# Performance work log

Hardware: AMD Instinct MI355X
Metric: run time of the kernel (lower is better)

Reference implementation:

```python
import jax, jax.numpy as jnp
import numpy as np

N_E = 8192
E_DIM = 256
BETA = 0.25


def setup_inputs() -> dict:
    key = jax.random.key(0)
    k1, k2 = jax.random.split(key)
    z = jax.random.normal(k1, (4, 256, 16, 16, 16), dtype=jnp.float32)
    weight = jax.random.normal(k2, (N_E, E_DIM), dtype=jnp.float32)
    return {"z": z, "weight": weight}


def reference(z, weight):
    # b c l h w -> b l h w c
    zc = jnp.transpose(z, (0, 2, 3, 4, 1))
    zf = zc.reshape(-1, E_DIM)  # [N, D]
    n = zf.shape[0]

    # squared euclidean distances to all codes: [N, n_e]
    d = (jnp.sum(zf * zf, axis=1, keepdims=True)
         + jnp.sum(weight * weight, axis=1)
         - 2.0 * jnp.einsum('bd,nd->bn', zf, weight))
    idx = jnp.argmin(d, axis=1)  # [N] int

    z_q = weight[idx].reshape(zc.shape)  # codebook gather

    # histogram of code usage (equivalent to one-hot mean, without the NxK one-hot)
    counts = jnp.zeros((N_E,), dtype=zf.dtype).at[idx].add(1.0)
    avg_probs = counts / jnp.asarray(n, zf.dtype)
    perplexity = jnp.exp(-jnp.sum(avg_probs * jnp.log(avg_probs + 1e-10)))
    unique = jnp.sum(counts > 0).astype(jnp.int32)

    # commitment loss (z_q detached) + straight-through estimator
    loss = BETA * jnp.mean((jax.lax.stop_gradient(z_q) - zc) ** 2)
    z_q_st = zc + jax.lax.stop_gradient(z_q - zc)

    # b l h w c -> b c l h w
    z_q_out = jnp.transpose(z_q_st, (0, 4, 1, 2, 3))
    return z_q_out, loss, perplexity, unique, idx
```

## Files before the change

kernel.cpp:

```cpp
#include <hip/hip_runtime.h>

#define NQ     16384
#define EDIM   256
#define NE     8192
#define LHW    4096
#define BETA   0.25f

#define WS_WSQ    0
#define WS_CNT    32768
#define WS_LOSS   65536
#define WS_IDX    65792
#define WS_BEST   131328
#define WS_APACK  2359552
#define WS_BPACK  10748160
#define WS_NEED   14942464

typedef __attribute__((ext_vector_type(8))) short bf16x8;
typedef __attribute__((ext_vector_type(4))) float f32x4;

__device__ __forceinline__ unsigned f32_sortable(float f) {
    unsigned b = __float_as_uint(f);
    return b ^ ((unsigned)((int)b >> 31) | 0x80000000u);
}
__device__ __forceinline__ unsigned short bf16_rn(float f) {
    unsigned u = __float_as_uint(f);
    return (unsigned short)((u + 0x7FFFu + ((u >> 16) & 1u)) >> 16);
}

__global__ __launch_bounds__(256) void wsq_pack_w(const float* __restrict__ w,
                                                  float* __restrict__ wsq,
                                                  unsigned* __restrict__ Bp32,
                                                  unsigned* __restrict__ counts,
                                                  float* __restrict__ loss) {
    int wave = threadIdx.x >> 6, lane = threadIdx.x & 63;
    int row = blockIdx.x * 4 + wave;
    if (blockIdx.x < 32) {
        counts[blockIdx.x * 256 + threadIdx.x] = 0u;
        if (blockIdx.x == 0 && threadIdx.x == 0) loss[0] = 0.f;
    }
    float4 v = *(const float4*)(w + (size_t)row * EDIM + lane * 4);
    double s = (double)v.x * v.x + (double)v.y * v.y +
               (double)v.z * v.z + (double)v.w * v.w;
    unsigned p0 = (unsigned)bf16_rn(v.x) | ((unsigned)bf16_rn(v.y) << 16);
    unsigned p1 = (unsigned)bf16_rn(v.z) | ((unsigned)bf16_rn(v.w) << 16);
    *(uint2*)(Bp32 + (size_t)row * 128 + lane * 2) = make_uint2(p0, p1);
    #pragma unroll
    for (int off = 32; off; off >>= 1) s += __shfl_xor(s, off, 64);
    if (lane == 0) wsq[row] = (float)s;
}

__global__ __launch_bounds__(256) void wsq_kernel(const float* __restrict__ w,
                                                  float* __restrict__ wsq) {
    int wave = threadIdx.x >> 6, lane = threadIdx.x & 63;
    int row = blockIdx.x * 4 + wave;
    float4 v = *(const float4*)(w + (size_t)row * EDIM + lane * 4);
    double s = (double)v.x * v.x + (double)v.y * v.y +
               (double)v.z * v.z + (double)v.w * v.w;
    #pragma unroll
    for (int off = 32; off; off >>= 1) s += __shfl_xor(s, off, 64);
    if (lane == 0) wsq[row] = (float)s;
}

__global__ __launch_bounds__(1024) void pack_z(const float* __restrict__ z,
                                               unsigned* __restrict__ Ap32) {
    __shared__ unsigned lds[64 * 129];
    int tid = threadIdx.x;
    int tn = tid & 63, tc = tid >> 6;
    int n0 = blockIdx.x * 64;
    int n = n0 + tn;
    int b = n >> 12, lhw = n & 4095;
    #pragma unroll
    for (int cc = 0; cc < 16; cc += 2) {
        int d = tc * 16 + cc;
        float v0 = z[((size_t)b * EDIM + d) * LHW + lhw];
        float v1 = z[((size_t)b * EDIM + d + 1) * LHW + lhw];
        lds[tn * 129 + (d >> 1)] =
            (unsigned)bf16_rn(v0) | ((unsigned)bf16_rn(v1) << 16);
    }
    __syncthreads();
    #pragma unroll
    for (int p = 0; p < 8; ++p) {
        int flat = p * 1024 + tid;
        int row = flat >> 7, c = flat & 127;
        Ap32[(size_t)(n0 + row) * 128 + c] = lds[row * 129 + c];
    }
}

__global__ __launch_bounds__(256, 3) void dist_mfma(const unsigned short* __restrict__ Ap,
                                                    const unsigned short* __restrict__ Bp,
                                                    const float* __restrict__ wsq,
                                                    unsigned* __restrict__ s1) {
    __shared__ __align__(16) unsigned short lds_b[2][128 * 64];
    int tid = threadIdx.x, lane = tid & 63, w = tid >> 6;
    int x = blockIdx.x, nt = blockIdx.y;
    int quad = lane >> 4, col = lane & 15;
    int rsel = lane >> 3, seg = lane & 7;

    const unsigned short* arow = Ap + (size_t)(nt * 128 + w * 32 + col) * 256;
    const unsigned short* Bbase = Bp + (size_t)(x * 128) * 256;

    f32x4 acc[2][8];
    #pragma unroll
    for (int i = 0; i < 2; ++i)
        #pragma unroll
        for (int j = 0; j < 8; ++j) acc[i][j] = (f32x4){0.f, 0.f, 0.f, 0.f};

    auto stage_chunk = [&](int kc, int bsel) {
        int k0s = kc * 64;
        #pragma unroll
        for (int p = 0; p < 4; ++p) {
            int c = w * 4 + p;
            const unsigned short* gb =
                Bbase + (size_t)(c * 8 + rsel) * 256 + k0s + ((seg ^ (rsel & 7)) * 8);
            __builtin_amdgcn_global_load_lds(
                (const __attribute__((address_space(1))) void*)gb,
                (__attribute__((address_space(3))) void*)(&lds_b[bsel][c * 512]),
                16, 0, 0);
        }
    };

    stage_chunk(0, 0);

    #pragma unroll
    for (int kcc = 0; kcc < 4; ++kcc) {
        int k0 = kcc * 64;
        int cur = kcc & 1;
        bf16x8 af[2][2];
        #pragma unroll
        for (int i = 0; i < 2; ++i)
            #pragma unroll
            for (int h = 0; h < 2; ++h)
                af[i][h] = *(const bf16x8*)(arow + i * 16 * 256 + k0 + h * 32 + quad * 8);
        asm volatile("" ::: "memory");
        if (kcc < 3) {
            stage_chunk(kcc + 1, cur ^ 1);
            asm volatile("s_waitcnt vmcnt(8)" ::: "memory");
        } else {
            asm volatile("s_waitcnt vmcnt(4)" ::: "memory");
        }
        __builtin_amdgcn_s_barrier();
        asm volatile("" ::: "memory");
        __builtin_amdgcn_s_setprio(1);
        #pragma unroll
        for (int h = 0; h < 2; ++h) {
            bf16x8 bf[8];
            #pragma unroll
            for (int j = 0; j < 8; ++j)
                bf[j] = *(const bf16x8*)(&lds_b[cur][(j * 16 + col) * 64 +
                                         (((h * 4 + quad) ^ (col & 7)) * 8)]);
            #pragma unroll
            for (int i = 0; i < 2; ++i)
                #pragma unroll
                for (int j = 0; j < 8; ++j)
                    acc[i][j] = __builtin_amdgcn_mfma_f32_16x16x32_bf16(
                        af[i][h], bf[j], acc[i][j], 0, 0, 0);
        }
        __builtin_amdgcn_s_setprio(0);
        asm volatile("" ::: "memory");
        if (kcc < 3) {
            __builtin_amdgcn_s_barrier();
            asm volatile("" ::: "memory");
        }
    }

    unsigned m1[2][4], m2[2][4];
    #pragma unroll
    for (int i = 0; i < 2; ++i)
        #pragma unroll
        for (int r = 0; r < 4; ++r) { m1[i][r] = 0xFFFFFFFFu; m2[i][r] = 0xFFFFFFFFu; }
    #pragma unroll
    for (int j = 0; j < 8; ++j) {
        int e = x * 128 + j * 16 + col;
        unsigned jc = (unsigned)(j * 16 + col);
        float wq_off = wsq[e] + 4096.0f;
        #pragma unroll
        for (int i = 0; i < 2; ++i)
            #pragma unroll
            for (int r = 0; r < 4; ++r) {
                float d = fmaf(-2.0f, acc[i][j][r], wq_off);
                unsigned k = (__float_as_uint(d) & 0xFFFFFF80u) | jc;
                unsigned mx = (m1[i][r] > k) ? m1[i][r] : k;
                m1[i][r] = (m1[i][r] < k) ? m1[i][r] : k;
                m2[i][r] = (m2[i][r] < mx) ? m2[i][r] : mx;
            }
    }
    #pragma unroll
    for (int i = 0; i < 2; ++i)
        #pragma unroll
        for (int r = 0; r < 4; ++r) {
            unsigned a1 = m1[i][r], a2 = m2[i][r];
            #pragma unroll
            for (int off = 1; off < 16; off <<= 1) {
                unsigned b1 = __shfl_xor(a1, off, 64);
                unsigned b2 = __shfl_xor(a2, off, 64);
                unsigned lo1 = a1 < b1 ? a1 : b1;
                unsigned hi1 = a1 < b1 ? b1 : a1;
                unsigned lo2 = a2 < b2 ? a2 : b2;
                a1 = lo1;
                a2 = hi1 < lo2 ? hi1 : lo2;
            }
            if (col == 0) {
                int q = nt * 128 + w * 32 + i * 16 + quad * 4 + r;
                size_t o = (size_t)q * 128 + x * 2;
                s1[o] = a1; s1[o + 1] = a2;
            }
        }
}

__global__ __launch_bounds__(256) void refine_kernel(const float* __restrict__ z,
                                                     const float* __restrict__ w,
                                                     const float* __restrict__ wsq,
                                                     const unsigned* __restrict__ s1,
                                                     unsigned* __restrict__ idxarr) {
    __shared__ float lds_z[4][260];
    int tid = threadIdx.x, lane = tid & 63, wv = tid >> 6;
    int q0 = blockIdx.x * 4;
    int q = q0 + wv;
    int b = q0 >> 12, lhw0 = q0 & 4095;
    {
        float4 zc = *(const float4*)(z + ((size_t)b * EDIM + tid) * LHW + lhw0);
        lds_z[0][tid] = zc.x; lds_z[1][tid] = zc.y;
        lds_z[2][tid] = zc.z; lds_z[3][tid] = zc.w;
    }
    uint2 kk2 = *(const uint2*)(s1 + (size_t)q * 128 + lane * 2);
    unsigned long long a1 =
        ((unsigned long long)(kk2.x >> 7) << 13) | (unsigned)(lane * 128 + (kk2.x & 127u));
    unsigned long long a2 =
        ((unsigned long long)(kk2.y >> 7) << 13) | (unsigned)(lane * 128 + (kk2.y & 127u));
    #pragma unroll
    for (int off = 1; off < 8; off <<= 1) {
        unsigned long long b1 = __shfl_xor(a1, off, 64);
        unsigned long long b2 = __shfl_xor(a2, off, 64);
        unsigned long long lo1 = a1 < b1 ? a1 : b1;
        unsigned long long hi1 = a1 < b1 ? b1 : a1;
        unsigned long long lo2 = a2 < b2 ? a2 : b2;
        a1 = lo1;
        a2 = hi1 < lo2 ? hi1 : lo2;
    }
    __syncthreads();
    float zv[4];
    #pragma unroll
    for (int t = 0; t < 4; ++t)
        zv[t] = lds_z[wv][lane * 4 + t];
    unsigned long long bestk = ~0ull;
    #pragma unroll
    for (int c = 0; c < 16; ++c) {
        int src = (c >> 1) * 8;
        unsigned long long kc = (c & 1) ? __shfl(a2, src, 64) : __shfl(a1, src, 64);
        unsigned e = (unsigned)(kc & (unsigned long long)(NE - 1));
        float4 wv4 = *(const float4*)(w + (size_t)e * EDIM + lane * 4);
        float p = zv[0] * wv4.x + zv[1] * wv4.y + zv[2] * wv4.z + zv[3] * wv4.w;
        #pragma unroll
        for (int off = 32; off; off >>= 1) p += __shfl_xor(p, off, 64);
        float d = wsq[e] - 2.0f * p;
        unsigned long long key = ((unsigned long long)f32_sortable(d) << 32) | e;
        if (key < bestk) bestk = key;
    }
    if (lane == 0) idxarr[q] = (unsigned)(bestk & 0xFFFFFFFFull);
}

__global__ __launch_bounds__(256, 2) void dist_fp32(const float* __restrict__ z,
                                                    const float* __restrict__ w,
                                                    const float* __restrict__ wsq,
                                                    unsigned long long* __restrict__ best) {
    __shared__ float lds_a[32 * 128];
    __shared__ float lds_b[32 * 132];
    int tid = threadIdx.x;
    int tx = tid & 15, ty = tid >> 4;
    int n0 = blockIdx.y * 128;
    int bb_ = n0 >> 12, lhw0 = n0 & 4095;
    const float* zb = z + (size_t)bb_ * (EDIM * LHW) + lhw0;
    int ebase = blockIdx.x * 2048;
    unsigned long long runmin[8];
    #pragma unroll
    for (int i = 0; i < 8; ++i) runmin[i] = ~0ull;
    float acc[64];
    for (int et = 0; et < 16; ++et) {
        int e0 = ebase + et * 128;
        #pragma unroll
        for (int i = 0; i < 64; ++i) acc[i] = 0.f;
        for (int kc = 0; kc < 8; ++kc) {
            int k0 = kc * 32;
            #pragma unroll
            for (int p = 0; p < 4; ++p) {
                int f = p * 256 + tid;
                int kk = f >> 5, nn4 = f & 31;
                float4 v = *(const float4*)(zb + (size_t)(k0 + kk) * LHW + nn4 * 4);
                *((float4*)(lds_a + kk * 128 + nn4 * 4)) = v;
            }
            #pragma unroll
            for (int p = 0; p < 4; ++p) {
                int f = p * 256 + tid;
                int ee = f >> 3, kk4 = f & 7;
                float4 v = *(const float4*)(w + (size_t)(e0 + ee) * EDIM + k0 + kk4 * 4);
                lds_b[(kk4 * 4 + 0) * 132 + ee] = v.x;
                lds_b[(kk4 * 4 + 1) * 132 + ee] = v.y;
                lds_b[(kk4 * 4 + 2) * 132 + ee] = v.z;
                lds_b[(kk4 * 4 + 3) * 132 + ee] = v.w;
            }
            __syncthreads();
            #pragma unroll
            for (int k = 0; k < 32; ++k) {
                float a[8], bv[8];
                *(float4*)(a)      = *(float4*)(lds_a + k * 128 + ty * 8);
                *(float4*)(a + 4)  = *(float4*)(lds_a + k * 128 + ty * 8 + 4);
                *(float4*)(bv)     = *(float4*)(lds_b + k * 132 + tx * 8);
                *(float4*)(bv + 4) = *(float4*)(lds_b + k * 132 + tx * 8 + 4);
                #pragma unroll
                for (int i = 0; i < 8; ++i)
                    #pragma unroll
                    for (int j = 0; j < 8; ++j)
                        acc[i * 8 + j] = fmaf(a[i], bv[j], acc[i * 8 + j]);
            }
            __syncthreads();
        }
        #pragma unroll
        for (int i = 0; i < 8; ++i) {
            unsigned long long m = runmin[i];
            #pragma unroll
            for (int j = 0; j < 8; ++j) {
                int e = e0 + tx * 8 + j;
                float d = wsq[e] - 2.0f * acc[i * 8 + j];
                unsigned long long key =
                    ((unsigned long long)f32_sortable(d) << 32) | (unsigned)e;
                m = (m < key) ? m : key;
            }
            runmin[i] = m;
        }
    }
    #pragma unroll
    for (int i = 0; i < 8; ++i) {
        unsigned long long kk = runmin[i];
        #pragma unroll
        for (int off = 8; off >= 1; off >>= 1) {
            unsigned long long o = __shfl_xor(kk, off, 16);
            kk = (kk < o) ? kk : o;
        }
        if (tx == 0) atomicMin(&best[n0 + ty * 8 + i], kk);
    }
}

__global__ __launch_bounds__(256) void extract_idx(const unsigned long long* __restrict__ best,
                                                   unsigned* __restrict__ idxarr) {
    int n = blockIdx.x * 256 + threadIdx.x;
    idxarr[n] = (unsigned)(best[n] & 0xFFFFFFFFull) & (NE - 1);
}

__global__ __launch_bounds__(1024) void gather_kernel(const float* __restrict__ z,
                                                      const float* __restrict__ w,
                                                      const unsigned* __restrict__ idxarr,
                                                      unsigned* __restrict__ counts,
                                                      float* __restrict__ loss,
                                                      float* __restrict__ out,
                                                      float* __restrict__ out_idx) {
    __shared__ int idx_s[64];
    __shared__ float wl[64 * 257];
    __shared__ float lsum[16];
    int tid = threadIdx.x;
    int n0 = blockIdx.x * 64;
    if (tid < 64) {
        int idx = (int)(idxarr[n0 + tid] & (NE - 1));
        idx_s[tid] = idx;
        out_idx[n0 + tid] = (float)idx;
        atomicAdd(&counts[idx], 1u);
    }
    __syncthreads();
    {
        int r0 = tid >> 8, cl = tid & 255;
        #pragma unroll
        for (int i = 0; i < 16; ++i)
            wl[(r0 + i * 4) * 257 + cl] = w[(size_t)idx_s[r0 + i * 4] * EDIM + cl];
    }
    __syncthreads();
    int tn = tid & 63, tc = tid >> 6;
    int bb_ = n0 >> 12, lhw0 = n0 & 4095;
    size_t zb = (size_t)bb_ * (EDIM * LHW) + lhw0 + tn;
    float accl = 0.f;
    #pragma unroll
    for (int cc = 0; cc < 16; ++cc) {
        int c = tc * 16 + cc;
        float wv = wl[tn * 257 + c];
        size_t a = zb + (size_t)c * LHW;
        float zv = z[a];
        float diff = wv - zv;
        out[a] = zv + diff;
        accl += diff * diff;
    }
    #pragma unroll
    for (int off = 32; off; off >>= 1) accl += __shfl_xor(accl, off, 64);
    if ((tid & 63) == 0) lsum[tid >> 6] = accl;
    __syncthreads();
    if (tid < 16) {
        float v = lsum[tid];
        v += __shfl_xor(v, 8, 16);
        v += __shfl_xor(v, 4, 16);
        v += __shfl_xor(v, 2, 16);
        v += __shfl_xor(v, 1, 16);
        if (tid == 0) atomicAdd(loss, v);
    }
}

__global__ __launch_bounds__(256) void finalize_kernel(const unsigned* __restrict__ counts,
                                                       const float* __restrict__ loss,
                                                       float* __restrict__ out_scalars) {
    __shared__ float ss[4];
    __shared__ int uu[4];
    int tid = threadIdx.x;
    float s = 0.f;
    int uniq = 0;
    for (int i = tid; i < NE; i += 256) {
        unsigned c = counts[i];
        if (c > 0) {
            float p = (float)c * (1.0f / (float)NQ);
            s += p * logf(p + 1e-10f);
            uniq++;
        }
    }
    #pragma unroll
    for (int off = 32; off; off >>= 1) {
        s += __shfl_xor(s, off, 64);
        uniq += __shfl_xor(uniq, off, 64);
    }
    int wave = tid >> 6;
    if ((tid & 63) == 0) { ss[wave] = s; uu[wave] = uniq; }
    __syncthreads();
    if (tid == 0) {
        float st = ss[0] + ss[1] + ss[2] + ss[3];
        int ut = uu[0] + uu[1] + uu[2] + uu[3];
        out_scalars[0] = BETA * loss[0] * (1.0f / (float)(NQ * EDIM));
        out_scalars[1] = expf(-st);
        out_scalars[2] = (float)ut;
    }
}

extern "C" void kernel_launch(void* const* d_in, const int* in_sizes, int n_in,
                              void* d_out, int out_size, void* d_ws, size_t ws_size,
                              hipStream_t stream) {
    const float* z = (const float*)d_in[0];
    const float* w = (const float*)d_in[1];
    float* out = (float*)d_out;
    char* ws = (char*)d_ws;
    float* wsq = (float*)(ws + WS_WSQ);
    unsigned* counts = (unsigned*)(ws + WS_CNT);
    float* loss = (float*)(ws + WS_LOSS);
    unsigned* idxarr = (unsigned*)(ws + WS_IDX);
    unsigned long long* best = (unsigned long long*)(ws + WS_BEST);
    unsigned* Ap = (unsigned*)(ws + WS_APACK);
    unsigned* Bp = (unsigned*)(ws + WS_BPACK);

    int idx_off = out_size - NQ;
    int scal_off = idx_off - 3;
    float* out_idx = out + idx_off;
    float* out_scalars = out + scal_off;

    unsigned* s1 = (unsigned*)out;

    if (ws_size >= (size_t)WS_NEED) {
        wsq_pack_w<<<NE / 4, 256, 0, stream>>>(w, wsq, Bp, counts, loss);
        pack_z<<<NQ / 64, 1024, 0, stream>>>(z, Ap);
        dist_mfma<<<dim3(64, 128), 256, 0, stream>>>((const unsigned short*)Ap,
                                                     (const unsigned short*)Bp, wsq, s1);
        refine_kernel<<<NQ / 4, 256, 0, stream>>>(z, w, wsq, s1, idxarr);
    } else {
        hipMemsetAsync(counts, 0, NE * sizeof(unsigned), stream);
        hipMemsetAsync(loss, 0, sizeof(float), stream);
        wsq_kernel<<<NE / 4, 256, 0, stream>>>(w, wsq);
        hipMemsetAsync(best, 0xFF, NQ * sizeof(unsigned long long), stream);
        dist_fp32<<<dim3(4, 128), 256, 0, stream>>>(z, w, wsq, best);
        extract_idx<<<NQ / 256, 256, 0, stream>>>(best, idxarr);
    }

    gather_kernel<<<NQ / 64, 1024, 0, stream>>>(z, w, idxarr, counts, loss, out, out_idx);
    finalize_kernel<<<1, 256, 0, stream>>>(counts, loss, out_scalars);
}
```

Baseline: 237.8 us.

## Process four codebook tiles per block, overlapping argmin epilogue with next tile's MFMAs

Each dist_mfma block now walks four consecutive 128-code tiles instead of one, with double-buffered accumulators so the top-2 selection and shuffle merge of the previous tile are interleaved with the MFMA loop of the current tile. B-tile staging is pipelined continuously across tile boundaries, and the grid shrinks from 64 to 16 blocks in x. The aim is to hide the epilogue's ALU and shuffle work and the per-block ramp-up behind matrix-core work. The cost is doubled accumulator registers, which lowers the occupancy target from 3 to 2 blocks and leaves fewer blocks to fill the GPU.

```diff
diff --git a/kernel.cpp b/kernel.cpp
--- a/kernel.cpp
+++ b/kernel.cpp
@@ -86,32 +86,28 @@
     }
 }
 
-__global__ __launch_bounds__(256, 3) void dist_mfma(const unsigned short* __restrict__ Ap,
+__global__ __launch_bounds__(256, 2) void dist_mfma(const unsigned short* __restrict__ Ap,
                                                     const unsigned short* __restrict__ Bp,
                                                     const float* __restrict__ wsq,
                                                     unsigned* __restrict__ s1) {
     __shared__ __align__(16) unsigned short lds_b[2][128 * 64];
     int tid = threadIdx.x, lane = tid & 63, w = tid >> 6;
-    int x = blockIdx.x, nt = blockIdx.y;
+    int xg = blockIdx.x, nt = blockIdx.y;
     int quad = lane >> 4, col = lane & 15;
     int rsel = lane >> 3, seg = lane & 7;
 
     const unsigned short* arow = Ap + (size_t)(nt * 128 + w * 32 + col) * 256;
-    const unsigned short* Bbase = Bp + (size_t)(x * 128) * 256;
-
-    f32x4 acc[2][8];
-    #pragma unroll
-    for (int i = 0; i < 2; ++i)
-        #pragma unroll
-        for (int j = 0; j < 8; ++j) acc[i][j] = (f32x4){0.f, 0.f, 0.f, 0.f};
-
-    auto stage_chunk = [&](int kc, int bsel) {
-        int k0s = kc * 64;
+
+    f32x4 accA[2][8], accB[2][8];
+    unsigned m1[2][4], m2[2][4];
+    float wqA[8], wqB[8];
+
+    auto stage = [&](int xt, int kc, int bsel) {
         #pragma unroll
         for (int p = 0; p < 4; ++p) {
             int c = w * 4 + p;
-            const unsigned short* gb =
-                Bbase + (size_t)(c * 8 + rsel) * 256 + k0s + ((seg ^ (rsel & 7)) * 8);
+            const unsigned short* gb = Bp + (size_t)(xt * 128 + c * 8 + rsel) * 256
+                                       + kc * 64 + ((seg ^ (rsel & 7)) * 8);
             __builtin_amdgcn_global_load_lds(
                 (const __attribute__((address_space(1))) void*)gb,
                 (__attribute__((address_space(3))) void*)(&lds_b[bsel][c * 512]),
@@ -119,92 +115,134 @@
         }
     };
 
-    stage_chunk(0, 0);
-
-    #pragma unroll
-    for (int kcc = 0; kcc < 4; ++kcc) {
-        int k0 = kcc * 64;
-        int cur = kcc & 1;
-        bf16x8 af[2][2];
+    auto slice2 = [&](const f32x4 (&ap)[2][8], const float (&wqp)[8],
+                      int jbase, bool first) {
+        if (first) {
+            #pragma unroll
+            for (int i = 0; i < 2; ++i)
+                #pragma unroll
+                for (int r = 0; r < 4; ++r) { m1[i][r] = 0xFFFFFFFFu; m2[i][r] = 0xFFFFFFFFu; }
+        }
+        #pragma unroll
+        for (int jo = 0; jo < 2; ++jo) {
+            int jj = jbase + jo;
+            unsigned jc = (unsigned)(jj * 16 + col);
+            float wq = wqp[jj] + 4096.0f;
+            #pragma unroll
+            for (int i = 0; i < 2; ++i)
+                #pragma unroll
+                for (int r = 0; r < 4; ++r) {
+                    float d = fmaf(-2.0f, ap[i][jj][r], wq);
+                    unsigned kk = (__float_as_uint(d) & 0xFFFFFF80u) | jc;
+                    unsigned mx = (m1[i][r] > kk) ? m1[i][r] : kk;
+                    m1[i][r] = (m1[i][r] < kk) ? m1[i][r] : kk;
+                    m2[i][r] = (m2[i][r] < mx) ? m2[i][r] : mx;
+                }
+        }
+    };
+
+    auto merge_write = [&](int xt) {
         #pragma unroll
         for (int i = 0; i < 2; ++i)
             #pragma unroll
-            for (int h = 0; h < 2; ++h)
-                af[i][h] = *(const bf16x8*)(arow + i * 16 * 256 + k0 + h * 32 + quad * 8);
-        asm volatile("" ::: "memory");
-        if (kcc < 3) {
-            stage_chunk(kcc + 1, cur ^ 1);
-            asm volatile("s_waitcnt vmcnt(8)" ::: "memory");
-        } else {
-            asm volatile("s_waitcnt vmcnt(4)" ::: "memory");
-        }
-        __builtin_amdgcn_s_barrier();
-        asm volatile("" ::: "memory");
-        __builtin_amdgcn_s_setprio(1);
-        #pragma unroll
-        for (int h = 0; h < 2; ++h) {
-            bf16x8 bf[8];
-            #pragma unroll
-            for (int j = 0; j < 8; ++j)
-                bf[j] = *(const bf16x8*)(&lds_b[cur][(j * 16 + col) * 64 +
-                                         (((h * 4 + quad) ^ (col & 7)) * 8)]);
+            for (int r = 0; r < 4; ++r) {
+                unsigned a1 = m1[i][r], a2 = m2[i][r];
+                #pragma unroll
+                for (int off = 1; off < 16; off <<= 1) {
+                    unsigned b1 = __shfl_xor(a1, off, 64);
+                    unsigned b2 = __shfl_xor(a2, off, 64);
+                    unsigned lo1 = a1 < b1 ? a1 : b1;
+                    unsigned hi1 = a1 < b1 ? b1 : a1;
+                    unsigned lo2 = a2 < b2 ? a2 : b2;
+                    a1 = lo1;
+                    a2 = hi1 < lo2 ? hi1 : lo2;
+                }
+                if (col == 0) {
+                    int q = nt * 128 + w * 32 + i * 16 + quad * 4 + r;
+                    size_t o = (size_t)q * 128 + xt * 2;
+                    s1[o] = a1; s1[o + 1] = a2;
+                }
+            }
+    };
+
+    stage(xg * 4, 0, 0);
+
+    #pragma unroll
+    for (int t = 0; t < 4; ++t) {
+        f32x4 (&acc)[2][8]  = (t & 1) ? accB : accA;
+        f32x4 (&accp)[2][8] = (t & 1) ? accA : accB;
+        float (&wqc)[8] = (t & 1) ? wqB : wqA;
+        float (&wqp)[8] = (t & 1) ? wqA : wqB;
+        int xt = xg * 4 + t;
+        #pragma unroll
+        for (int k = 0; k < 4; ++k) {
+            int p = t * 4 + k, cur = p & 1;
+            if (k == 0) {
+                #pragma unroll
+                for (int i = 0; i < 2; ++i)
+                    #pragma unroll
+                    for (int j = 0; j < 8; ++j) acc[i][j] = (f32x4){0.f, 0.f, 0.f, 0.f};
+            }
+            bf16x8 af[2][2];
             #pragma unroll
             for (int i = 0; i < 2; ++i)
                 #pragma unroll
+                for (int h = 0; h < 2; ++h)
+                    af[i][h] = *(const bf16x8*)(arow + i * 16 * 256 + k * 64 + h * 32 + quad * 8);
+            asm volatile("" ::: "memory");
+            if (k == 3) {
+                #pragma unroll
                 for (int j = 0; j < 8; ++j)
-                    acc[i][j] = __builtin_amdgcn_mfma_f32_16x16x32_bf16(
-                        af[i][h], bf[j], acc[i][j], 0, 0, 0);
-        }
-        __builtin_amdgcn_s_setprio(0);
-        asm volatile("" ::: "memory");
-        if (kcc < 3) {
+                    wqc[j] = wsq[xt * 128 + j * 16 + col];
+                asm volatile("" ::: "memory");
+            }
+            bool last = (t == 3 && k == 3);
+            if (!last) {
+                int t2 = (k == 3) ? t + 1 : t;
+                int k2 = (k == 3) ? 0 : k + 1;
+                stage(xg * 4 + t2, k2, cur ^ 1);
+            }
+            asm volatile("" ::: "memory");
+            if (k == 3) {
+                if (t == 3) asm volatile("s_waitcnt vmcnt(12)" ::: "memory");
+                else        asm volatile("s_waitcnt vmcnt(16)" ::: "memory");
+            } else {
+                asm volatile("s_waitcnt vmcnt(8)" ::: "memory");
+            }
             __builtin_amdgcn_s_barrier();
             asm volatile("" ::: "memory");
-        }
-    }
-
-    unsigned m1[2][4], m2[2][4];
-    #pragma unroll
-    for (int i = 0; i < 2; ++i)
-        #pragma unroll
-        for (int r = 0; r < 4; ++r) { m1[i][r] = 0xFFFFFFFFu; m2[i][r] = 0xFFFFFFFFu; }
-    #pragma unroll
-    for (int j = 0; j < 8; ++j) {
-        int e = x * 128 + j * 16 + col;
-        unsigned jc = (unsigned)(j * 16 + col);
-        float wq_off = wsq[e] + 4096.0f;
-        #pragma unroll
-        for (int i = 0; i < 2; ++i)
-            #pragma unroll
-            for (int r = 0; r < 4; ++r) {
-                float d = fmaf(-2.0f, acc[i][j][r], wq_off);
-                unsigned k = (__float_as_uint(d) & 0xFFFFFF80u) | jc;
-                unsigned mx = (m1[i][r] > k) ? m1[i][r] : k;
-                m1[i][r] = (m1[i][r] < k) ? m1[i][r] : k;
-                m2[i][r] = (m2[i][r] < mx) ? m2[i][r] : mx;
-            }
-    }
-    #pragma unroll
-    for (int i = 0; i < 2; ++i)
-        #pragma unroll
-        for (int r = 0; r < 4; ++r) {
-            unsigned a1 = m1[i][r], a2 = m2[i][r];
-            #pragma unroll
-            for (int off = 1; off < 16; off <<= 1) {
-                unsigned b1 = __shfl_xor(a1, off, 64);
-                unsigned b2 = __shfl_xor(a2, off, 64);
-                unsigned lo1 = a1 < b1 ? a1 : b1;
-                unsigned hi1 = a1 < b1 ? b1 : a1;
-                unsigned lo2 = a2 < b2 ? a2 : b2;
-                a1 = lo1;
-                a2 = hi1 < lo2 ? hi1 : lo2;
-            }
-            if (col == 0) {
-                int q = nt * 128 + w * 32 + i * 16 + quad * 4 + r;
-                size_t o = (size_t)q * 128 + x * 2;
-                s1[o] = a1; s1[o + 1] = a2;
-            }
-        }
+            __builtin_amdgcn_s_setprio(1);
+            #pragma unroll
+            for (int h = 0; h < 2; ++h) {
+                bf16x8 bf[8];
+                #pragma unroll
+                for (int j = 0; j < 8; ++j)
+                    bf[j] = *(const bf16x8*)(&lds_b[cur][(j * 16 + col) * 64 +
+                                             (((h * 4 + quad) ^ (col & 7)) * 8)]);
+                #pragma unroll
+                for (int i = 0; i < 2; ++i)
+                    #pragma unroll
+                    for (int j = 0; j < 8; ++j)
+                        acc[i][j] = __builtin_amdgcn_mfma_f32_16x16x32_bf16(
+                            af[i][h], bf[j], acc[i][j], 0, 0, 0);
+            }
+            __builtin_amdgcn_s_setprio(0);
+            if (t > 0) {
+                slice2(accp, wqp, k * 2, k == 0);
+                if (k == 3) merge_write(xt - 1);
+            }
+            __builtin_amdgcn_sched_barrier(0);
+            asm volatile("" ::: "memory");
+            if (!last) {
+                __builtin_amdgcn_s_barrier();
+                asm volatile("" ::: "memory");
+            }
+        }
+    }
+    #pragma unroll
+    for (int k = 0; k < 4; ++k)
+        slice2(accB, wqB, k * 2, k == 0);
+    merge_write(xg * 4 + 3);
 }
 
 __global__ __launch_bounds__(256) void refine_kernel(const float* __restrict__ z,
@@ -458,7 +496,7 @@
     if (ws_size >= (size_t)WS_NEED) {
         wsq_pack_w<<<NE / 4, 256, 0, stream>>>(w, wsq, Bp, counts, loss);
         pack_z<<<NQ / 64, 1024, 0, stream>>>(z, Ap);
-        dist_mfma<<<dim3(64, 128), 256, 0, stream>>>((const unsigned short*)Ap,
+        dist_mfma<<<dim3(16, 128), 256, 0, stream>>>((const unsigned short*)Ap,
                                                      (const unsigned short*)Bp, wsq, s1);
         refine_kernel<<<NQ / 4, 256, 0, stream>>>(z, w, wsq, s1, idxarr);
     } else {
```

Measured after the change: 266.9 us. +12.3%, slower.
